# Optimization experiments

Hardware: AMD Instinct MI355X
Metric: run time of the kernel (lower is better)

Reference implementation:

```python
import jax, jax.numpy as jnp
import numpy as np

NUM_HEADS = 16


def _rotate_half(x):
    x1, x2 = jnp.split(x, 2, axis=-1)
    return jnp.concatenate((-x2, x1), axis=-1)


def setup_inputs() -> dict:
    key = jax.random.key(0)
    ks = jax.random.split(key, 6)
    S, HID, D, W = 32768, 1280, 80, 64
    x = jax.random.normal(ks[0], (S, HID), dtype=jnp.float32)
    # rotary embeddings: use actual cos/sin of random phases for realism
    ang = jax.random.uniform(ks[1], (S, D), dtype=jnp.float32) * 6.28318
    cos = jnp.cos(ang)
    sin = jnp.sin(ang)
    # uniform windows of 64 tokens -> 512 windows
    cu_seqlens = (jnp.arange(S // W + 1, dtype=jnp.int32) * W)
    qkv_kernel = jax.random.normal(ks[2], (HID, 3 * HID), dtype=jnp.float32) * (HID ** -0.5)
    qkv_bias = jnp.zeros((3 * HID,), dtype=jnp.float32)
    proj_kernel = jax.random.normal(ks[3], (HID, HID), dtype=jnp.float32) * (HID ** -0.5)
    proj_bias = jnp.zeros((HID,), dtype=jnp.float32)
    return {"x": x, "cos": cos, "sin": sin, "cu_seqlens": cu_seqlens,
            "qkv_kernel": qkv_kernel, "qkv_bias": qkv_bias,
            "proj_kernel": proj_kernel, "proj_bias": proj_bias}


def reference(x, cos, sin, cu_seqlens, qkv_kernel, qkv_bias, proj_kernel, proj_bias):
    S, HID = x.shape
    H = NUM_HEADS
    D = HID // H
    scale = D ** -0.5

    qkv = x @ qkv_kernel + qkv_bias                      # [S, 3*HID]
    q, k, v = jnp.split(qkv, 3, axis=-1)
    q = q.reshape(S, H, D)
    k = k.reshape(S, H, D)
    v = v.reshape(S, H, D)

    c = cos[:, :D][:, None, :]                           # [S, 1, D]
    s = sin[:, :D][:, None, :]
    q = q * c + _rotate_half(q) * s
    k = k * c + _rotate_half(k) * s

    # Uniform windows: cu_seqlens = W * arange(nw+1); vectorize the per-window
    # full attention as a batched block-diagonal attention [nw, W, H, D].
    nw = cu_seqlens.shape[0] - 1
    W = S // nw
    qw = q.reshape(nw, W, H, D).astype(jnp.float32)
    kw = k.reshape(nw, W, H, D).astype(jnp.float32)
    vw = v.reshape(nw, W, H, D).astype(jnp.float32)

    scores = jnp.einsum('nqhd,nkhd->nhqk', qw, kw) * scale   # [nw, H, W, W]
    weights = jax.nn.softmax(scores, axis=-1)
    out = jnp.einsum('nhqk,nkhd->nqhd', weights, vw)          # [nw, W, H, D]
    out = out.reshape(S, HID).astype(x.dtype)
    return out @ proj_kernel + proj_bias
```

## Files before the change

kernel.cpp:

```cpp
#include <hip/hip_runtime.h>
#include <hip/hip_bf16.h>
#include <hip/hip_fp16.h>

typedef __attribute__((ext_vector_type(8))) short short8;
typedef __attribute__((ext_vector_type(4))) float f32x4;
typedef __attribute__((ext_vector_type(16))) float f32x16;
typedef unsigned short u16;
typedef unsigned int u32;

__device__ __forceinline__ u16 f2bf(float v) {
  __hip_bfloat16 h = __float2bfloat16(v);
  return __builtin_bit_cast(u16, h);
}
__device__ __forceinline__ float bf2f(u16 u) {
  return __builtin_bit_cast(float, (u32)u << 16);
}
__device__ __forceinline__ u16 f2h(float v) {
  __half h = __float2half(v);
  return __builtin_bit_cast(u16, h);
}
__device__ __forceinline__ float h2f(u16 u) {
  return __half2float(__builtin_bit_cast(__half, u));
}

__global__ __launch_bounds__(256) void casth(const float* __restrict__ X, long long n,
                                             u16* __restrict__ H) {
  long long i0 = ((long long)blockIdx.x * 256 + threadIdx.x) * 4;
  long long stride = (long long)gridDim.x * 256 * 4;
  for (long long i = i0; i < n; i += stride) {
    float4 v = *(const float4*)(X + i);
    ushort4 h;
    h.x = f2h(v.x);
    h.y = f2h(v.y);
    h.z = f2h(v.z);
    h.w = f2h(v.w);
    *(ushort4*)(H + i) = h;
  }
}

__global__ __launch_bounds__(256) void transpose_cast(const float* __restrict__ W,
    int K, int N, u16* __restrict__ T) {
  __shared__ float tile[64][65];
  const int nb = N >> 6;
  const int br = blockIdx.x / nb, bc = blockIdx.x - br * nb;
  const int tx = threadIdx.x & 63, ty = threadIdx.x >> 6;
  #pragma unroll
  for (int i = ty; i < 64; i += 4)
    tile[i][tx] = W[(size_t)(br * 64 + i) * N + bc * 64 + tx];
  __syncthreads();
  #pragma unroll
  for (int i = ty; i < 64; i += 4) {
    size_t off = (size_t)(bc * 64 + i) * K + br * 64 + tx;
    T[off] = f2h(tile[tx][i]);
  }
}

__global__ __launch_bounds__(256) void transpose_split(const float* __restrict__ W,
    int K, int N, u16* __restrict__ Thi, u16* __restrict__ Tlo) {
  __shared__ float tile[64][65];
  const int nb = N >> 6;
  const int br = blockIdx.x / nb, bc = blockIdx.x - br * nb;
  const int tx = threadIdx.x & 63, ty = threadIdx.x >> 6;
  #pragma unroll
  for (int i = ty; i < 64; i += 4)
    tile[i][tx] = W[(size_t)(br * 64 + i) * N + bc * 64 + tx];
  __syncthreads();
  #pragma unroll
  for (int i = ty; i < 64; i += 4) {
    float v = tile[tx][i];
    u16 hb = f2bf(v);
    size_t off = (size_t)(bc * 64 + i) * K + br * 64 + tx;
    Thi[off] = hb;
    Tlo[off] = f2bf(v - bf2f(hb));
  }
}

__global__ __launch_bounds__(256) void rope_qkb(u16* __restrict__ qkv,
    const float* __restrict__ cosg, const float* __restrict__ sing) {
  const int idx = blockIdx.x * 256 + threadIdx.x;
  const int row = idx / 80;
  const int rem = idx - row * 80;
  const int h = rem / 5;
  const int dd = (rem - h * 5) * 8;
  u16* qp = qkv + (size_t)row * 3840 + h * 80 + dd;
  u16* kp = qp + 1280;
  const float* cp = cosg + row * 80 + dd;
  const float* sp = sing + row * 80 + dd;
  short8 qa = *(short8*)qp,        qb = *(short8*)(qp + 40);
  short8 ka = *(short8*)kp,        kb = *(short8*)(kp + 40);
  f32x4 cL0 = *(const f32x4*)cp,        cL1 = *(const f32x4*)(cp + 4);
  f32x4 sL0 = *(const f32x4*)sp,        sL1 = *(const f32x4*)(sp + 4);
  f32x4 cH0 = *(const f32x4*)(cp + 40), cH1 = *(const f32x4*)(cp + 44);
  f32x4 sH0 = *(const f32x4*)(sp + 40), sH1 = *(const f32x4*)(sp + 44);
  short8 oqa, oqb, oka, okb;
  #pragma unroll
  for (int j = 0; j < 8; ++j) {
    float cl = j < 4 ? cL0[j] : cL1[j - 4];
    float sl = j < 4 ? sL0[j] : sL1[j - 4];
    float ch = j < 4 ? cH0[j] : cH1[j - 4];
    float sh = j < 4 ? sH0[j] : sH1[j - 4];
    float qaf = bf2f((u16)qa[j]), qbf = bf2f((u16)qb[j]);
    float kaf = bf2f((u16)ka[j]), kbf = bf2f((u16)kb[j]);
    oqa[j] = (short)f2bf(qaf * cl - qbf * sl);
    oqb[j] = (short)f2bf(qbf * ch + qaf * sh);
    oka[j] = (short)f2bf(kaf * cl - kbf * sl);
    okb[j] = (short)f2bf(kbf * ch + kaf * sh);
  }
  *(short8*)qp = oqa;        *(short8*)(qp + 40) = oqb;
  *(short8*)kp = oka;        *(short8*)(kp + 40) = okb;
}

__device__ __forceinline__ void gload16(const void* g, void* l) {
  __builtin_amdgcn_global_load_lds((const __attribute__((address_space(1))) u32*)g,
                                   (__attribute__((address_space(3))) u32*)l, 16, 0, 0);
}
__device__ __forceinline__ void mfma32b(f32x16& c, short8 a, short8 b) {
  asm("v_mfma_f32_32x32x16_bf16 %0, %1, %2, %0" : "+v"(c) : "v"(a), "v"(b));
}
__device__ __forceinline__ void mfma32h(f32x16& c, short8 a, short8 b) {
  asm("v_mfma_f32_32x32x16_f16 %0, %1, %2, %0" : "+v"(c) : "v"(a), "v"(b));
}

#define CFENCE() asm volatile("" ::: "memory")
#define BAR() do { CFENCE(); __builtin_amdgcn_s_barrier(); CFENCE(); } while (0)

#define HS0 0
#define HS1 32768
#define HS2 65536

#define STAGEH(t_, sb_) do {                                                   \
  const size_t go__ = (size_t)srow * 1280 + (size_t)(t_) * 32 + skoff;         \
  char* l__ = smem + (sb_) + tid * 16;                                         \
  gload16(Ap + go__,      l__);                                                \
  gload16(Ap + go__ + 16, l__ + 8192);                                         \
  gload16(Bp + go__,      l__ + 16384);                                        \
  gload16(Bp + go__ + 16, l__ + 24576);                                        \
} while (0)

#define PHH(q_, sC_, sS_, vm4_, st_) do {                                      \
  if (vm4_) asm volatile("s_waitcnt vmcnt(4)" ::: "memory");                   \
  else      asm volatile("s_waitcnt vmcnt(0)" ::: "memory");                   \
  BAR();                                                                       \
  if (st_) STAGEH((q_) + 2, sS_);                                              \
  _Pragma("unroll")                                                            \
  for (int kk = 0; kk < 2; ++kk) {                                             \
    const char* hb__ = smem + (sC_) + kk * 8192;                               \
    short8 ah__[4], bh__[2];                                                   \
    _Pragma("unroll")                                                          \
    for (int m = 0; m < 4; ++m)                                                \
      ah__[m] = *(const short8*)(hb__ + ((wm4 + m) << 10) + laneOff);          \
    _Pragma("unroll")                                                          \
    for (int n = 0; n < 2; ++n)                                                \
      bh__[n] = *(const short8*)(hb__ + 16384 + ((wn2 + n) << 10) + laneOff);  \
    __builtin_amdgcn_s_setprio(1);                                             \
    _Pragma("unroll")                                                          \
    for (int m = 0; m < 4; ++m)                                                \
      _Pragma("unroll")                                                        \
      for (int n = 0; n < 2; ++n) mfma32h(acc[m][n], ah__[m], bh__[n]);        \
    __builtin_amdgcn_s_setprio(0);                                             \
  }                                                                            \
} while (0)

__global__ __launch_bounds__(512, 2) void gemmhb(
    const u16* __restrict__ A, const u16* __restrict__ B,
    const float* __restrict__ bias, u16* __restrict__ Cout, int N) {
  __shared__ char smem[98304];
  const int tid = threadIdx.x;
  const int lane = tid & 63;
  const int l31 = lane & 31, h = lane >> 5;
  const int wave = tid >> 6;
  const int wm = wave >> 2, wn = wave & 3;
  const int wm4 = wm * 4, wn2 = wn * 2;
  const int nwg = gridDim.x;
  int tile = ((int)blockIdx.x & 7) * (nwg >> 3) + ((int)blockIdx.x >> 3);
  const int ntn = N >> 8;
  const int bm = tile / ntn, bn = tile - bm * ntn;

  const int lr = lane & 15;
  const int laneOff = ((lr >> 1) << 7) +
                      ((((((lane & 1) << 2) | (lane >> 4)) ^ (lr >> 1)) & 7) << 4);
  const int cell = tid & 63, line = cell >> 3, slotc = cell & 7;
  const int uu = slotc ^ line;
  const int lam = (uu >> 2) | (line << 1) | ((uu & 3) << 4);
  const int srow = ((tid >> 6) << 5) + (lam & 31);
  const int skoff = (lam >> 5) << 3;

  const u16* Ap = A + (size_t)bm * 256 * 1280;
  const u16* Bp = B + (size_t)bn * 256 * 1280;

  f32x16 acc[4][2];
  #pragma unroll
  for (int m = 0; m < 4; ++m)
    #pragma unroll
    for (int n = 0; n < 2; ++n)
      #pragma unroll
      for (int j = 0; j < 16; ++j) acc[m][n][j] = 0.f;

  STAGEH(0, HS0);
  STAGEH(1, HS1);

  #pragma unroll 1
  for (int g = 0; g < 12; ++g) {
    const int q = 3 * g;
    PHH(q,     HS0, HS2, 1, 1);
    PHH(q + 1, HS1, HS0, 1, 1);
    PHH(q + 2, HS2, HS1, 1, 1);
  }
  PHH(36, HS0, HS2, 1, 1);
  PHH(37, HS1, HS0, 1, 1);
  PHH(38, HS2, HS1, 1, 0);
  PHH(39, HS0, HS1, 0, 0);

  asm volatile("s_nop 7\ns_nop 7\ns_nop 7");
  #pragma unroll
  for (int n = 0; n < 2; ++n) {
    const int col = bn * 256 + wn * 64 + n * 32 + l31;
    const float bv = bias[col];
    #pragma unroll
    for (int m = 0; m < 4; ++m) {
      const int rbase = bm * 256 + wm * 128 + m * 32 + 4 * h;
      #pragma unroll
      for (int rr = 0; rr < 16; ++rr) {
        const int grow = rbase + (rr & 3) + 8 * (rr >> 2);
        Cout[(size_t)grow * N + col] = f2bf(acc[m][n][rr] + bv);
      }
    }
  }
}

#define PS0 0
#define PS1 32768
#define PS2 65536

#define STAGEP(t_, sb_) do {                                                   \
  const size_t go__ = (size_t)srow * 1280 + (size_t)(t_) * 32 + skoff;         \
  char* l__ = smem + (sb_) + tid * 16;                                         \
  gload16(Ap + go__,      l__);                                                \
  gload16(Ap + go__ + 16, l__ + 8192);                                         \
  gload16(Bp + go__,      l__ + 16384);                                        \
  gload16(Bp + go__ + 16, l__ + 24576);                                        \
} while (0)

#define PHP(q_, sC_, sS_, vm4_, st_) do {                                      \
  if (vm4_) asm volatile("s_waitcnt vmcnt(4)" ::: "memory");                   \
  else      asm volatile("s_waitcnt vmcnt(0)" ::: "memory");                   \
  BAR();                                                                       \
  if (st_) STAGEP((q_) + 2, sS_);                                              \
  _Pragma("unroll")                                                            \
  for (int kk = 0; kk < 2; ++kk) {                                             \
    const char* hb__ = smem + (sC_) + kk * 8192;                               \
    short8 ah__[4], bh__[2];                                                   \
    _Pragma("unroll")                                                          \
    for (int m = 0; m < 4; ++m)                                                \
      ah__[m] = *(const short8*)(hb__ + ((wm4 + m) << 10) + laneOff);          \
    _Pragma("unroll")                                                          \
    for (int n = 0; n < 2; ++n)                                                \
      bh__[n] = *(const short8*)(hb__ + 16384 + ((wn2 + n) << 10) + laneOff);  \
    __builtin_amdgcn_s_setprio(1);                                             \
    _Pragma("unroll")                                                          \
    for (int m = 0; m < 4; ++m)                                                \
      _Pragma("unroll")                                                        \
      for (int n = 0; n < 2; ++n) mfma32b(acc[m][n], ah__[m], bh__[n]);        \
    __builtin_amdgcn_s_setprio(0);                                             \
  }                                                                            \
} while (0)

__global__ __launch_bounds__(512, 2) void gemmp1(
    const u16* __restrict__ A, const u16* __restrict__ B,
    const float* __restrict__ bias, float* __restrict__ Cout, int N) {
  __shared__ char smem[98304];
  const int tid = threadIdx.x;
  const int lane = tid & 63;
  const int l31 = lane & 31, h = lane >> 5;
  const int wave = tid >> 6;
  const int wm = wave >> 2, wn = wave & 3;
  const int wm4 = wm * 4, wn2 = wn * 2;
  const int nwg = gridDim.x;
  int tile = ((int)blockIdx.x & 7) * (nwg >> 3) + ((int)blockIdx.x >> 3);
  const int ntn = N >> 8;
  const int bm = tile / ntn, bn = tile - bm * ntn;

  const int lr = lane & 15;
  const int laneOff = ((lr >> 1) << 7) +
                      ((((((lane & 1) << 2) | (lane >> 4)) ^ (lr >> 1)) & 7) << 4);
  const int cell = tid & 63, line = cell >> 3, slotc = cell & 7;
  const int uu = slotc ^ line;
  const int lam = (uu >> 2) | (line << 1) | ((uu & 3) << 4);
  const int srow = ((tid >> 6) << 5) + (lam & 31);
  const int skoff = (lam >> 5) << 3;

  const u16* Ap = A + (size_t)bm * 256 * 1280;
  const u16* Bp = B + (size_t)bn * 256 * 1280;

  f32x16 acc[4][2];
  #pragma unroll
  for (int m = 0; m < 4; ++m)
    #pragma unroll
    for (int n = 0; n < 2; ++n)
      #pragma unroll
      for (int j = 0; j < 16; ++j) acc[m][n][j] = 0.f;

  STAGEP(0, PS0);
  STAGEP(1, PS1);

  #pragma unroll 1
  for (int g = 0; g < 12; ++g) {
    const int q = 3 * g;
    PHP(q,     PS0, PS2, 1, 1);
    PHP(q + 1, PS1, PS0, 1, 1);
    PHP(q + 2, PS2, PS1, 1, 1);
  }
  PHP(36, PS0, PS2, 1, 1);
  PHP(37, PS1, PS0, 1, 1);
  PHP(38, PS2, PS1, 1, 0);
  PHP(39, PS0, PS1, 0, 0);

  asm volatile("s_nop 7\ns_nop 7\ns_nop 7");
  #pragma unroll
  for (int n = 0; n < 2; ++n) {
    const int col = bn * 256 + wn * 64 + n * 32 + l31;
    const float bv = bias[col];
    #pragma unroll
    for (int m = 0; m < 4; ++m) {
      const int rbase = bm * 256 + wm * 128 + m * 32 + 4 * h;
      #pragma unroll
      for (int rr = 0; rr < 16; ++rr) {
        const int grow = rbase + (rr & 3) + 8 * (rr >> 2);
        Cout[(size_t)grow * N + col] = acc[m][n][rr] + bv;
      }
    }
  }
}

#define ATT_SCALE 0.11180339887498949f
__global__ __launch_bounds__(256) void attn_win(const u16* __restrict__ qkv,
    u16* __restrict__ ohi) {
  __shared__ __attribute__((aligned(16))) u16 Qs[64 * 104];
  __shared__ __attribute__((aligned(16))) u16 Ks[64 * 104];
  __shared__ __attribute__((aligned(16))) u16 Vt[80 * 72];
  __shared__ __attribute__((aligned(16))) u16 Ps[64 * 72];
  const int t = threadIdx.x;
  const int w = blockIdx.x >> 4, h = blockIdx.x & 15;
  const int rowbase = w * 64;
  const int wave = t >> 6, lane = t & 63;
  const int lr = lane & 15, lg = lane >> 4;

  for (int c = t; c < 64 * 12; c += 256) {
    int s = c / 12, d8 = c - s * 12;
    short8 q8 = (short8){0,0,0,0,0,0,0,0}, k8 = (short8){0,0,0,0,0,0,0,0};
    if (d8 < 10) {
      const u16* b = qkv + (size_t)(rowbase + s) * 3840 + h * 80 + d8 * 8;
      q8 = *(const short8*)b;
      k8 = *(const short8*)(b + 1280);
    }
    *(short8*)&Qs[s * 104 + d8 * 8] = q8;
    *(short8*)&Ks[s * 104 + d8 * 8] = k8;
  }
  for (int c = t; c < 640; c += 256) {
    int s = c / 10, d0 = (c - s * 10) * 8;
    short8 v = *(const short8*)(qkv + (size_t)(rowbase + s) * 3840 + 2560 + h * 80 + d0);
    #pragma unroll
    for (int j = 0; j < 8; ++j) Vt[(d0 + j) * 72 + s] = (u16)v[j];
  }
  __syncthreads();

  f32x4 sf[4];
  #pragma unroll
  for (int fc = 0; fc < 4; ++fc) sf[fc] = (f32x4){0.f, 0.f, 0.f, 0.f};
  #pragma unroll
  for (int kk = 0; kk < 3; ++kk) {
    short8 qf = *(const short8*)((const char*)Qs + (wave * 16 + lr) * 208 + kk * 64 + lg * 16);
    #pragma unroll
    for (int fc = 0; fc < 4; ++fc) {
      short8 kf = *(const short8*)((const char*)Ks + (fc * 16 + lr) * 208 + kk * 64 + lg * 16);
      asm("v_mfma_f32_16x16x32_bf16 %0, %1, %2, %0" : "+v"(sf[fc]) : "v"(qf), "v"(kf));
    }
  }
  asm volatile("s_nop 7\ns_nop 7");

  float pr[4][4];
  #pragma unroll
  for (int fc = 0; fc < 4; ++fc)
    #pragma unroll
    for (int j = 0; j < 4; ++j) pr[fc][j] = sf[fc][j] * ATT_SCALE;
  #pragma unroll
  for (int j = 0; j < 4; ++j) {
    float m = fmaxf(fmaxf(pr[0][j], pr[1][j]), fmaxf(pr[2][j], pr[3][j]));
    m = fmaxf(m, __shfl_xor(m, 1));
    m = fmaxf(m, __shfl_xor(m, 2));
    m = fmaxf(m, __shfl_xor(m, 4));
    m = fmaxf(m, __shfl_xor(m, 8));
    float sum = 0.f;
    #pragma unroll
    for (int fc = 0; fc < 4; ++fc) { pr[fc][j] = __expf(pr[fc][j] - m); sum += pr[fc][j]; }
    sum += __shfl_xor(sum, 1);
    sum += __shfl_xor(sum, 2);
    sum += __shfl_xor(sum, 4);
    sum += __shfl_xor(sum, 8);
    float inv = 1.f / sum;
    #pragma unroll
    for (int fc = 0; fc < 4; ++fc) pr[fc][j] *= inv;
  }
  #pragma unroll
  for (int j = 0; j < 4; ++j) {
    int row = wave * 16 + lg * 4 + j;
    #pragma unroll
    for (int fc = 0; fc < 4; ++fc) {
      u32 pb = (u32)f2bf(pr[fc][j]);
      u32 partner = (u32)__shfl_xor((int)pb, 1);
      if ((lr & 1) == 0)
        *(u32*)((char*)Ps + row * 144 + (fc * 16 + lr) * 2) = pb | (partner << 16);
    }
  }
  __syncthreads();

  f32x4 av[5];
  #pragma unroll
  for (int fd = 0; fd < 5; ++fd) av[fd] = (f32x4){0.f, 0.f, 0.f, 0.f};
  #pragma unroll
  for (int kk = 0; kk < 2; ++kk) {
    short8 pf = *(const short8*)((const char*)Ps + (wave * 16 + lr) * 144 + kk * 64 + lg * 16);
    #pragma unroll
    for (int fd = 0; fd < 5; ++fd) {
      short8 vf = *(const short8*)((const char*)Vt + (fd * 16 + lr) * 144 + kk * 64 + lg * 16);
      asm("v_mfma_f32_16x16x32_bf16 %0, %1, %2, %0" : "+v"(av[fd]) : "v"(pf), "v"(vf));
    }
  }
  asm volatile("s_nop 7\ns_nop 7");

  #pragma unroll
  for (int fd = 0; fd < 5; ++fd)
    #pragma unroll
    for (int j = 0; j < 4; ++j) {
      int grow = rowbase + wave * 16 + lg * 4 + j;
      size_t off = (size_t)grow * 1280 + h * 80 + fd * 16 + lr;
      ohi[off] = f2bf(av[fd][j]);
    }
}

extern "C" void kernel_launch(void* const* d_in, const int* in_sizes, int n_in,
                              void* d_out, int out_size, void* d_ws, size_t ws_size,
                              hipStream_t stream) {
  const float* x     = (const float*)d_in[0];
  const float* cosg  = (const float*)d_in[1];
  const float* sing  = (const float*)d_in[2];
  const float* wqkv  = (const float*)d_in[4];
  const float* bqkv  = (const float*)d_in[5];
  const float* wproj = (const float*)d_in[6];
  const float* bproj = (const float*)d_in[7];
  float* out = (float*)d_out;

  char* ws = (char*)d_ws;
  const size_t SZ_QKV = 251658240ull;
  const size_t SZ_X   = 83886080ull;
  const size_t SZ_WQ  = 9830400ull;
  const size_t SZ_WP  = 3276800ull;
  u16* qkv  = (u16*)(ws);
  u16* xh   = (u16*)(ws + SZ_QKV);
  u16* abf  = (u16*)(ws + SZ_QKV + SZ_X);
  u16* wqt  = (u16*)(ws + SZ_QKV + 2 * SZ_X);
  u16* wpth = (u16*)(ws + SZ_QKV + 2 * SZ_X + SZ_WQ);
  u16* wptl = (u16*)(ws + SZ_QKV + 2 * SZ_X + SZ_WQ + SZ_WP);
  if (ws_size < SZ_QKV + 2 * SZ_X + SZ_WQ + 2 * SZ_WP) return;

  casth<<<2048, 256, 0, stream>>>(x, 41943040ll, xh);
  transpose_cast<<<1200, 256, 0, stream>>>(wqkv, 1280, 3840, wqt);
  transpose_split<<<400, 256, 0, stream>>>(wproj, 1280, 1280, wpth, wptl);
  gemmhb<<<1920, 512, 0, stream>>>(xh, wqt, bqkv, qkv, 3840);
  rope_qkb<<<10240, 256, 0, stream>>>(qkv, cosg, sing);
  attn_win<<<8192, 256, 0, stream>>>(qkv, abf);
  gemmp1<<<640, 512, 0, stream>>>(abf, wpth, bproj, out, 1280);
}
```

Baseline: 799.9 us.

## Replace 256x256 pipelined GEMMs with simpler 128x128 single-buffered 16x16 MFMA GEMMs

```diff
diff --git a/kernel.cpp b/kernel.cpp
--- a/kernel.cpp
+++ b/kernel.cpp
@@ -4,7 +4,6 @@
 
 typedef __attribute__((ext_vector_type(8))) short short8;
 typedef __attribute__((ext_vector_type(4))) float f32x4;
-typedef __attribute__((ext_vector_type(16))) float f32x16;
 typedef unsigned short u16;
 typedef unsigned int u32;
 
@@ -55,8 +54,8 @@
   }
 }
 
-__global__ __launch_bounds__(256) void transpose_split(const float* __restrict__ W,
-    int K, int N, u16* __restrict__ Thi, u16* __restrict__ Tlo) {
+__global__ __launch_bounds__(256) void transpose_castb(const float* __restrict__ W,
+    int K, int N, u16* __restrict__ T) {
   __shared__ float tile[64][65];
   const int nb = N >> 6;
   const int br = blockIdx.x / nb, bc = blockIdx.x - br * nb;
@@ -67,11 +66,8 @@
   __syncthreads();
   #pragma unroll
   for (int i = ty; i < 64; i += 4) {
-    float v = tile[tx][i];
-    u16 hb = f2bf(v);
     size_t off = (size_t)(bc * 64 + i) * K + br * 64 + tx;
-    Thi[off] = hb;
-    Tlo[off] = f2bf(v - bf2f(hb));
+    T[off] = f2bf(tile[tx][i]);
   }
 }
 
@@ -114,221 +110,99 @@
   __builtin_amdgcn_global_load_lds((const __attribute__((address_space(1))) u32*)g,
                                    (__attribute__((address_space(3))) u32*)l, 16, 0, 0);
 }
-__device__ __forceinline__ void mfma32b(f32x16& c, short8 a, short8 b) {
-  asm("v_mfma_f32_32x32x16_bf16 %0, %1, %2, %0" : "+v"(c) : "v"(a), "v"(b));
-}
-__device__ __forceinline__ void mfma32h(f32x16& c, short8 a, short8 b) {
-  asm("v_mfma_f32_32x32x16_f16 %0, %1, %2, %0" : "+v"(c) : "v"(a), "v"(b));
-}
-
-#define CFENCE() asm volatile("" ::: "memory")
-#define BAR() do { CFENCE(); __builtin_amdgcn_s_barrier(); CFENCE(); } while (0)
-
-#define HS0 0
-#define HS1 32768
-#define HS2 65536
-
-#define STAGEH(t_, sb_) do {                                                   \
-  const size_t go__ = (size_t)srow * 1280 + (size_t)(t_) * 32 + skoff;         \
-  char* l__ = smem + (sb_) + tid * 16;                                         \
-  gload16(Ap + go__,      l__);                                                \
-  gload16(Ap + go__ + 16, l__ + 8192);                                         \
-  gload16(Bp + go__,      l__ + 16384);                                        \
-  gload16(Bp + go__ + 16, l__ + 24576);                                        \
-} while (0)
-
-#define PHH(q_, sC_, sS_, vm4_, st_) do {                                      \
-  if (vm4_) asm volatile("s_waitcnt vmcnt(4)" ::: "memory");                   \
-  else      asm volatile("s_waitcnt vmcnt(0)" ::: "memory");                   \
-  BAR();                                                                       \
-  if (st_) STAGEH((q_) + 2, sS_);                                              \
+
+
+#define G128_BODY(MFMA_INSN)                                                   \
+  __shared__ char smem[32768];                                                 \
+  const int tid = threadIdx.x;                                                 \
+  const int lane = tid & 63, wave = tid >> 6;                                  \
+  const int nwg = gridDim.x;                                                   \
+  int tile = ((int)blockIdx.x & 7) * (nwg >> 3) + ((int)blockIdx.x >> 3);      \
+  const int ntn = N >> 7;                                                      \
+  const int bm = tile / ntn, bn = tile - bm * ntn;                             \
+  const int wm = wave >> 1, wn = wave & 1;                                     \
+  const int lr = lane & 15, lg = lane >> 4;                                    \
+  f32x4 acc[4][4];                                                             \
   _Pragma("unroll")                                                            \
-  for (int kk = 0; kk < 2; ++kk) {                                             \
-    const char* hb__ = smem + (sC_) + kk * 8192;                               \
-    short8 ah__[4], bh__[2];                                                   \
+  for (int i = 0; i < 4; ++i)                                                  \
     _Pragma("unroll")                                                          \
-    for (int m = 0; m < 4; ++m)                                                \
-      ah__[m] = *(const short8*)(hb__ + ((wm4 + m) << 10) + laneOff);          \
+    for (int j = 0; j < 4; ++j) acc[i][j] = (f32x4){0.f, 0.f, 0.f, 0.f};       \
+  const char* Ab = (const char*)(A + (size_t)(bm * 128) * 1280);               \
+  const char* Bb = (const char*)(B + (size_t)(bn * 128) * 1280);               \
+  _Pragma("unroll 1")                                                          \
+  for (int kk = 0; kk < 20; ++kk) {                                            \
+    __syncthreads();                                                           \
     _Pragma("unroll")                                                          \
-    for (int n = 0; n < 2; ++n)                                                \
-      bh__[n] = *(const short8*)(hb__ + 16384 + ((wn2 + n) << 10) + laneOff);  \
-    __builtin_amdgcn_s_setprio(1);                                             \
+    for (int r4 = 0; r4 < 4; ++r4) {                                           \
+      int o = r4 * 4096 + wave * 1024 + lane * 16;                             \
+      int row = o >> 7;                                                        \
+      int cb = (o ^ ((row & 7) << 4)) & 127;                                   \
+      gload16(Ab + (size_t)row * 2560 + kk * 128 + cb,                         \
+              smem + r4 * 4096 + wave * 1024);                                 \
+      gload16(Bb + (size_t)row * 2560 + kk * 128 + cb,                         \
+              smem + 16384 + r4 * 4096 + wave * 1024);                         \
+    }                                                                          \
+    __syncthreads();                                                           \
+    short8 bfr[2][4];                                                          \
     _Pragma("unroll")                                                          \
-    for (int m = 0; m < 4; ++m)                                                \
+    for (int ks = 0; ks < 2; ++ks)                                             \
       _Pragma("unroll")                                                        \
-      for (int n = 0; n < 2; ++n) mfma32h(acc[m][n], ah__[m], bh__[n]);        \
-    __builtin_amdgcn_s_setprio(0);                                             \
+      for (int ni = 0; ni < 4; ++ni) {                                         \
+        int row = wn * 64 + ni * 16 + lr;                                      \
+        int slot = (ks * 4 + lg) ^ (row & 7);                                  \
+        bfr[ks][ni] = *(const short8*)(smem + 16384 + row * 128 + slot * 16);  \
+      }                                                                        \
+    _Pragma("unroll")                                                          \
+    for (int mi = 0; mi < 4; ++mi) {                                           \
+      int row = wm * 64 + mi * 16 + lr;                                        \
+      int s0 = lg ^ (row & 7);                                                 \
+      int s1 = (4 + lg) ^ (row & 7);                                           \
+      short8 a0 = *(const short8*)(smem + row * 128 + s0 * 16);                \
+      short8 a1 = *(const short8*)(smem + row * 128 + s1 * 16);                \
+      _Pragma("unroll")                                                        \
+      for (int ni = 0; ni < 4; ++ni) {                                         \
+        asm(MFMA_INSN " %0, %1, %2, %0" : "+v"(acc[mi][ni])                    \
+            : "v"(a0), "v"(bfr[0][ni]));                                       \
+        asm(MFMA_INSN " %0, %1, %2, %0" : "+v"(acc[mi][ni])                    \
+            : "v"(a1), "v"(bfr[1][ni]));                                       \
+      }                                                                        \
+    }                                                                          \
   }                                                                            \
-} while (0)
-
-__global__ __launch_bounds__(512, 2) void gemmhb(
+  asm volatile("s_nop 7\ns_nop 7\ns_nop 7");
+
+__global__ __launch_bounds__(256) void g128h(
     const u16* __restrict__ A, const u16* __restrict__ B,
     const float* __restrict__ bias, u16* __restrict__ Cout, int N) {
-  __shared__ char smem[98304];
-  const int tid = threadIdx.x;
-  const int lane = tid & 63;
-  const int l31 = lane & 31, h = lane >> 5;
-  const int wave = tid >> 6;
-  const int wm = wave >> 2, wn = wave & 3;
-  const int wm4 = wm * 4, wn2 = wn * 2;
-  const int nwg = gridDim.x;
-  int tile = ((int)blockIdx.x & 7) * (nwg >> 3) + ((int)blockIdx.x >> 3);
-  const int ntn = N >> 8;
-  const int bm = tile / ntn, bn = tile - bm * ntn;
-
-  const int lr = lane & 15;
-  const int laneOff = ((lr >> 1) << 7) +
-                      ((((((lane & 1) << 2) | (lane >> 4)) ^ (lr >> 1)) & 7) << 4);
-  const int cell = tid & 63, line = cell >> 3, slotc = cell & 7;
-  const int uu = slotc ^ line;
-  const int lam = (uu >> 2) | (line << 1) | ((uu & 3) << 4);
-  const int srow = ((tid >> 6) << 5) + (lam & 31);
-  const int skoff = (lam >> 5) << 3;
-
-  const u16* Ap = A + (size_t)bm * 256 * 1280;
-  const u16* Bp = B + (size_t)bn * 256 * 1280;
-
-  f32x16 acc[4][2];
-  #pragma unroll
-  for (int m = 0; m < 4; ++m)
-    #pragma unroll
-    for (int n = 0; n < 2; ++n)
+  G128_BODY("v_mfma_f32_16x16x32_f16")
+  #pragma unroll
+  for (int ni = 0; ni < 4; ++ni) {
+    int col = bn * 128 + wn * 64 + ni * 16 + lr;
+    float bv = bias[col];
+    #pragma unroll
+    for (int mi = 0; mi < 4; ++mi)
       #pragma unroll
-      for (int j = 0; j < 16; ++j) acc[m][n][j] = 0.f;
-
-  STAGEH(0, HS0);
-  STAGEH(1, HS1);
-
-  #pragma unroll 1
-  for (int g = 0; g < 12; ++g) {
-    const int q = 3 * g;
-    PHH(q,     HS0, HS2, 1, 1);
-    PHH(q + 1, HS1, HS0, 1, 1);
-    PHH(q + 2, HS2, HS1, 1, 1);
-  }
-  PHH(36, HS0, HS2, 1, 1);
-  PHH(37, HS1, HS0, 1, 1);
-  PHH(38, HS2, HS1, 1, 0);
-  PHH(39, HS0, HS1, 0, 0);
-
-  asm volatile("s_nop 7\ns_nop 7\ns_nop 7");
-  #pragma unroll
-  for (int n = 0; n < 2; ++n) {
-    const int col = bn * 256 + wn * 64 + n * 32 + l31;
-    const float bv = bias[col];
-    #pragma unroll
-    for (int m = 0; m < 4; ++m) {
-      const int rbase = bm * 256 + wm * 128 + m * 32 + 4 * h;
-      #pragma unroll
-      for (int rr = 0; rr < 16; ++rr) {
-        const int grow = rbase + (rr & 3) + 8 * (rr >> 2);
-        Cout[(size_t)grow * N + col] = f2bf(acc[m][n][rr] + bv);
+      for (int j = 0; j < 4; ++j) {
+        int r = bm * 128 + wm * 64 + mi * 16 + lg * 4 + j;
+        Cout[(size_t)r * N + col] = f2bf(acc[mi][ni][j] + bv);
       }
-    }
-  }
-}
-
-#define PS0 0
-#define PS1 32768
-#define PS2 65536
-
-#define STAGEP(t_, sb_) do {                                                   \
-  const size_t go__ = (size_t)srow * 1280 + (size_t)(t_) * 32 + skoff;         \
-  char* l__ = smem + (sb_) + tid * 16;                                         \
-  gload16(Ap + go__,      l__);                                                \
-  gload16(Ap + go__ + 16, l__ + 8192);                                         \
-  gload16(Bp + go__,      l__ + 16384);                                        \
-  gload16(Bp + go__ + 16, l__ + 24576);                                        \
-} while (0)
-
-#define PHP(q_, sC_, sS_, vm4_, st_) do {                                      \
-  if (vm4_) asm volatile("s_waitcnt vmcnt(4)" ::: "memory");                   \
-  else      asm volatile("s_waitcnt vmcnt(0)" ::: "memory");                   \
-  BAR();                                                                       \
-  if (st_) STAGEP((q_) + 2, sS_);                                              \
-  _Pragma("unroll")                                                            \
-  for (int kk = 0; kk < 2; ++kk) {                                             \
-    const char* hb__ = smem + (sC_) + kk * 8192;                               \
-    short8 ah__[4], bh__[2];                                                   \
-    _Pragma("unroll")                                                          \
-    for (int m = 0; m < 4; ++m)                                                \
-      ah__[m] = *(const short8*)(hb__ + ((wm4 + m) << 10) + laneOff);          \
-    _Pragma("unroll")                                                          \
-    for (int n = 0; n < 2; ++n)                                                \
-      bh__[n] = *(const short8*)(hb__ + 16384 + ((wn2 + n) << 10) + laneOff);  \
-    __builtin_amdgcn_s_setprio(1);                                             \
-    _Pragma("unroll")                                                          \
-    for (int m = 0; m < 4; ++m)                                                \
-      _Pragma("unroll")                                                        \
-      for (int n = 0; n < 2; ++n) mfma32b(acc[m][n], ah__[m], bh__[n]);        \
-    __builtin_amdgcn_s_setprio(0);                                             \
-  }                                                                            \
-} while (0)
-
-__global__ __launch_bounds__(512, 2) void gemmp1(
+  }
+}
+
+__global__ __launch_bounds__(256) void g128p(
     const u16* __restrict__ A, const u16* __restrict__ B,
     const float* __restrict__ bias, float* __restrict__ Cout, int N) {
-  __shared__ char smem[98304];
-  const int tid = threadIdx.x;
-  const int lane = tid & 63;
-  const int l31 = lane & 31, h = lane >> 5;
-  const int wave = tid >> 6;
-  const int wm = wave >> 2, wn = wave & 3;
-  const int wm4 = wm * 4, wn2 = wn * 2;
-  const int nwg = gridDim.x;
-  int tile = ((int)blockIdx.x & 7) * (nwg >> 3) + ((int)blockIdx.x >> 3);
-  const int ntn = N >> 8;
-  const int bm = tile / ntn, bn = tile - bm * ntn;
-
-  const int lr = lane & 15;
-  const int laneOff = ((lr >> 1) << 7) +
-                      ((((((lane & 1) << 2) | (lane >> 4)) ^ (lr >> 1)) & 7) << 4);
-  const int cell = tid & 63, line = cell >> 3, slotc = cell & 7;
-  const int uu = slotc ^ line;
-  const int lam = (uu >> 2) | (line << 1) | ((uu & 3) << 4);
-  const int srow = ((tid >> 6) << 5) + (lam & 31);
-  const int skoff = (lam >> 5) << 3;
-
-  const u16* Ap = A + (size_t)bm * 256 * 1280;
-  const u16* Bp = B + (size_t)bn * 256 * 1280;
-
-  f32x16 acc[4][2];
-  #pragma unroll
-  for (int m = 0; m < 4; ++m)
-    #pragma unroll
-    for (int n = 0; n < 2; ++n)
+  G128_BODY("v_mfma_f32_16x16x32_bf16")
+  #pragma unroll
+  for (int ni = 0; ni < 4; ++ni) {
+    int col = bn * 128 + wn * 64 + ni * 16 + lr;
+    float bv = bias[col];
+    #pragma unroll
+    for (int mi = 0; mi < 4; ++mi)
       #pragma unroll
-      for (int j = 0; j < 16; ++j) acc[m][n][j] = 0.f;
-
-  STAGEP(0, PS0);
-  STAGEP(1, PS1);
-
-  #pragma unroll 1
-  for (int g = 0; g < 12; ++g) {
-    const int q = 3 * g;
-    PHP(q,     PS0, PS2, 1, 1);
-    PHP(q + 1, PS1, PS0, 1, 1);
-    PHP(q + 2, PS2, PS1, 1, 1);
-  }
-  PHP(36, PS0, PS2, 1, 1);
-  PHP(37, PS1, PS0, 1, 1);
-  PHP(38, PS2, PS1, 1, 0);
-  PHP(39, PS0, PS1, 0, 0);
-
-  asm volatile("s_nop 7\ns_nop 7\ns_nop 7");
-  #pragma unroll
-  for (int n = 0; n < 2; ++n) {
-    const int col = bn * 256 + wn * 64 + n * 32 + l31;
-    const float bv = bias[col];
-    #pragma unroll
-    for (int m = 0; m < 4; ++m) {
-      const int rbase = bm * 256 + wm * 128 + m * 32 + 4 * h;
-      #pragma unroll
-      for (int rr = 0; rr < 16; ++rr) {
-        const int grow = rbase + (rr & 3) + 8 * (rr >> 2);
-        Cout[(size_t)grow * N + col] = acc[m][n][rr] + bv;
+      for (int j = 0; j < 4; ++j) {
+        int r = bm * 128 + wm * 64 + mi * 16 + lg * 4 + j;
+        Cout[(size_t)r * N + col] = acc[mi][ni][j] + bv;
       }
-    }
   }
 }
 
@@ -459,15 +333,14 @@
   u16* xh   = (u16*)(ws + SZ_QKV);
   u16* abf  = (u16*)(ws + SZ_QKV + SZ_X);
   u16* wqt  = (u16*)(ws + SZ_QKV + 2 * SZ_X);
-  u16* wpth = (u16*)(ws + SZ_QKV + 2 * SZ_X + SZ_WQ);
-  u16* wptl = (u16*)(ws + SZ_QKV + 2 * SZ_X + SZ_WQ + SZ_WP);
-  if (ws_size < SZ_QKV + 2 * SZ_X + SZ_WQ + 2 * SZ_WP) return;
+  u16* wpt  = (u16*)(ws + SZ_QKV + 2 * SZ_X + SZ_WQ);
+  if (ws_size < SZ_QKV + 2 * SZ_X + SZ_WQ + SZ_WP) return;
 
   casth<<<2048, 256, 0, stream>>>(x, 41943040ll, xh);
   transpose_cast<<<1200, 256, 0, stream>>>(wqkv, 1280, 3840, wqt);
-  transpose_split<<<400, 256, 0, stream>>>(wproj, 1280, 1280, wpth, wptl);
-  gemmhb<<<1920, 512, 0, stream>>>(xh, wqt, bqkv, qkv, 3840);
+  transpose_castb<<<400, 256, 0, stream>>>(wproj, 1280, 1280, wpt);
+  g128h<<<7680, 256, 0, stream>>>(xh, wqt, bqkv, qkv, 3840);
   rope_qkb<<<10240, 256, 0, stream>>>(qkv, cosg, sing);
   attn_win<<<8192, 256, 0, stream>>>(qkv, abf);
-  gemmp1<<<640, 512, 0, stream>>>(abf, wpth, bproj, out, 1280);
-}
+  g128p<<<2560, 256, 0, stream>>>(abf, wpt, bproj, out, 1280);
+}
```

Result: faster. 762.5 us (-4.7%).
